# Performance work log

Measured on AMD Instinct MI355X. Metric: run time of the kernel, lower is better.

## Reference

```python
import jax, jax.numpy as jnp
import numpy as np

N_NODES = 16384
DIM = 1024
NUM_HEADS = 16
HEAD_DIM = 64
CURV = -1.0  # hyperbolic stereographic (Poincare ball) curvature, shared by all heads
EPS = 1e-15
PROJ_EPS = 4e-3  # geoopt float32 projection eps


def _clamp_abs(x, eps):
    # geoopt.utils.clamp_abs: sign-preserving clamp of |x| (sign(0) -> +1)
    s = jnp.sign(jnp.sign(x) + 0.5)
    return s * jnp.maximum(jnp.abs(x), eps)


def _artan_k(x, k):  # k < 0: artanh(sqrt(-k) x)/sqrt(-k)
    sk = jnp.sqrt(jnp.maximum(jnp.abs(k), EPS))
    return jnp.arctanh(jnp.clip(sk * x, -1.0 + 1e-7, 1.0 - 1e-7)) / sk


def _tan_k(x, k):  # k < 0: tanh(sqrt(-k) x)/sqrt(-k)
    sk = jnp.sqrt(jnp.maximum(jnp.abs(k), EPS))
    return jnp.tanh(sk * x) / sk


def _norm(x):
    return jnp.maximum(jnp.linalg.norm(x, axis=-1, keepdims=True), EPS)


def _project(x, k):
    maxnorm = (1.0 - PROJ_EPS) / jnp.sqrt(jnp.maximum(jnp.abs(k), EPS))
    n = _norm(x)
    return jnp.where(n > maxnorm, x / n * maxnorm, x)


def _mobius_scalar_mul(r, x, k):
    xn = _norm(x)
    return _tan_k(r * _artan_k(xn, k), k) * x / xn


def _mobius_matvec(W, x, k):
    xn = _norm(x)
    mx = x @ W
    mxn = _norm(mx)
    res = _tan_k(mxn / xn * _artan_k(xn, k), k) * mx / mxn
    zero = jnp.all(mx == 0, axis=-1, keepdims=True)
    return jnp.where(zero, jnp.zeros((), x.dtype), res)


def _logmap0(y, k):
    yn = _norm(y)
    return _artan_k(yn, k) * y / yn


def _expmap0(u, k):
    un = _norm(u)
    return _project(_tan_k(un, k) * u / un, k)


def _kappa_relu(x, k):
    # manifold.apply(relu): relu in tangent space at origin
    return _expmap0(jax.nn.relu(_logmap0(x, k)), k)


def _geo_lin_attn(Q, K, V, mask, k):
    # Q,K,V: (H,N,hd); mask: (N,); k: (H,1,1)
    denom_pt = jnp.maximum(1.0 + k * jnp.sum(V * V, -1, keepdims=True), EPS)  # (H,N,1)
    v1 = jax.nn.elu(Q / denom_pt) + 1.0          # parallel_transport0back(V, Q) -> elu+1
    gamma = 2.0 / denom_pt                        # lambda_x(V)
    denominator = _clamp_abs(gamma - 1.0, 1e-10)
    m = mask[None, :, None]
    x = gamma / denominator * V * m
    v2 = denominator * (jax.nn.elu(K / denom_pt) + 1.0) * m
    v2_sum = jnp.sum(v2, axis=-2)                 # (H,hd)
    D = jnp.einsum('hnd,hd->hn', v1, v2_sum)
    D_inv = 1.0 / jnp.where(D == 0, 1e-5, D)
    context = jnp.einsum('hnd,hne->hde', v2, x)   # (H,hd,hd)
    out = jnp.einsum('hde,hnd,hn->hne', context, v1, D_inv)
    out = _project(out, k)
    out = _mobius_scalar_mul(0.5, out, k)
    return _project(out, k)


def setup_inputs():
    key = jax.random.key(0)
    ks = jax.random.split(key, 6)
    kc = jnp.float32(CURV)
    X = _project(0.02 * jax.random.normal(ks[0], (N_NODES, DIM), jnp.float32), kc)
    mask = jnp.ones((N_NODES,), jnp.float32)
    hdim = NUM_HEADS * HEAD_DIM
    Wq = 0.02 * jax.random.normal(ks[1], (DIM, hdim), jnp.float32)
    bq = jnp.zeros((hdim,), jnp.float32)
    Wk = 0.02 * jax.random.normal(ks[2], (DIM, hdim), jnp.float32)
    bk = jnp.zeros((hdim,), jnp.float32)
    Wv = 0.01 * jax.random.normal(ks[3], (DIM, hdim), jnp.float32)
    Wff = 0.01 * jax.random.normal(ks[4], (hdim, DIM), jnp.float32)
    return {"X": X, "mask": mask, "Wq": Wq, "bq": bq, "Wk": Wk, "bk": bk, "Wv": Wv, "Wff": Wff}


def reference(X, mask, Wq, bq, Wk, bk, Wv, Wff):
    kc = jnp.float32(CURV)
    k_head = jnp.full((NUM_HEADS, 1, 1), CURV, X.dtype)

    def split(t):  # (N, H*hd) -> (H, N, hd)
        return t.reshape(N_NODES, NUM_HEADS, HEAD_DIM).transpose(1, 0, 2)

    Q = split(X @ Wq + bq)
    K = split(X @ Wk + bk)
    V = split(_kappa_relu(_mobius_matvec(Wv, X, kc), kc))  # KappaGCN with A_hat=None
    attn = _geo_lin_attn(Q, K, V, mask, k_head)            # (H,N,hd)
    comb = attn.transpose(1, 0, 2).reshape(N_NODES, NUM_HEADS * HEAD_DIM)
    return _kappa_relu(_mobius_matvec(Wff, comb, kc), kc)
```

## Files before the change

### kernel.cpp

```cpp
#include <hip/hip_runtime.h>
#include <hip/hip_bf16.h>
#include <math.h>

#define N_NODES 16384
#define DIMV 1024
#define NHEADS 16
#define HEADD 64

typedef __attribute__((ext_vector_type(8))) short short8;
typedef __attribute__((ext_vector_type(4))) float f32x4;
typedef unsigned short ushort_t;

#define GLD16(gptr, lptr)                                                                 \
  __builtin_amdgcn_global_load_lds((const __attribute__((address_space(1))) void*)(gptr), \
                                   (__attribute__((address_space(3))) void*)(lptr), 16, 0, 0)


__device__ __forceinline__ float waveReduceSum(float v) {
#pragma unroll
  for (int m = 32; m; m >>= 1) v += __shfl_xor(v, m);
  return v;
}

__device__ __forceinline__ float blockReduceSum(float v, float* red) {
  float w = waveReduceSum(v);
  __syncthreads();
  if ((threadIdx.x & 63) == 0) red[threadIdx.x >> 6] = w;
  __syncthreads();
  return red[0] + red[1] + red[2] + red[3];
}

__device__ __forceinline__ float elup1_fast(float z) {
  return z > 0.0f ? z + 1.0f : __expf(z);
}

__device__ __forceinline__ float clampabs(float x, float eps) {
  float s = (x >= 0.0f) ? 1.0f : -1.0f;
  return s * fmaxf(fabsf(x), eps);
}

__device__ __forceinline__ ushort_t f2b(float x) {
  unsigned u = __float_as_uint(x);
  unsigned r = (u + 0x7FFFu + ((u >> 16) & 1u)) >> 16;
  return (ushort_t)r;
}
__device__ __forceinline__ float b2f(ushort_t h) {
  return __uint_as_float(((unsigned)h) << 16);
}

__global__ __launch_bounds__(256) void cvt_norm_kernel(const float* __restrict__ src,
                                                       ushort_t* __restrict__ dst,
                                                       float* __restrict__ rowsq) {
  __shared__ float red[4];
  const int row = blockIdx.x;
  const int t = threadIdx.x;
  float4 x4 = ((const float4*)(src + (size_t)row * DIMV))[t];
  ushort_t h[4] = {f2b(x4.x), f2b(x4.y), f2b(x4.z), f2b(x4.w)};
  ((uint2*)(dst + (size_t)row * DIMV))[t] = *(uint2*)h;
  float s = x4.x * x4.x + x4.y * x4.y + x4.z * x4.z + x4.w * x4.w;
  s = blockReduceSum(s, red);
  if (t == 0) rowsq[row] = s;
}

__global__ __launch_bounds__(256) void transW_kernel(const float* __restrict__ src,
                                                     ushort_t* __restrict__ hi) {
  __shared__ float tile[32][33];
  const int bx = blockIdx.x * 32, by = blockIdx.y * 32;
  const int tx = threadIdx.x & 31, ty = threadIdx.x >> 5;
#pragma unroll
  for (int i = 0; i < 32; i += 8) tile[ty + i][tx] = src[(size_t)(by + ty + i) * DIMV + bx + tx];
  __syncthreads();
#pragma unroll
  for (int i = 0; i < 32; i += 8)
    hi[(size_t)(bx + ty + i) * DIMV + by + tx] = f2b(tile[tx][ty + i]);
}

__global__ __launch_bounds__(256) void transW3_kernel(const float* __restrict__ s0,
                                                      const float* __restrict__ s1,
                                                      const float* __restrict__ s2,
                                                      ushort_t* __restrict__ d0,
                                                      ushort_t* __restrict__ d1,
                                                      ushort_t* __restrict__ d2) {
  __shared__ float tile[32][33];
  const float* src = (blockIdx.z == 0) ? s0 : (blockIdx.z == 1) ? s1 : s2;
  ushort_t* dst = (blockIdx.z == 0) ? d0 : (blockIdx.z == 1) ? d1 : d2;
  const int bx = blockIdx.x * 32, by = blockIdx.y * 32;
  const int tx = threadIdx.x & 31, ty = threadIdx.x >> 5;
#pragma unroll
  for (int i = 0; i < 32; i += 8) tile[ty + i][tx] = src[(size_t)(by + ty + i) * DIMV + bx + tx];
  __syncthreads();
#pragma unroll
  for (int i = 0; i < 32; i += 8)
    dst[(size_t)(bx + ty + i) * DIMV + by + tx] = f2b(tile[tx][ty + i]);
}


template <int EPI, int NB>
__global__ __launch_bounds__(512, 2) void gemm_bf(const ushort_t* __restrict__ A,
                                                  const ushort_t* __restrict__ Bt,
                                                  const float* __restrict__ biasQ,
                                                  const float* __restrict__ biasK,
                                                  const float* __restrict__ denom,
                                                  const float* __restrict__ mask,
                                                  float* __restrict__ v2sum,
                                                  float* __restrict__ mxhsq,
                                                  float* __restrict__ reluhsq,
                                                  ushort_t* __restrict__ Cq,
                                                  ushort_t* __restrict__ Ck) {
  __shared__ ushort_t As[2][256 * 64];
  __shared__ ushort_t Bs[2][256 * 64];
  const int bid = blockIdx.x;
  const int nwg = NB * 64;
  const int swz = (bid & 7) * (nwg / 8) + (bid >> 3);
  const int bm = (swz / NB) * 256;
  const int bn = (swz % NB) * 256;
  const int t = threadIdx.x;
  const int w = t >> 6, lane = t & 63, l15 = lane & 15;
  const int wr = (w >> 2) * 128;
  const int wcn = (w & 3) * 64;
  const int g4 = lane >> 4;
  const int e7 = l15 & 7;
  const int uo0 = (g4 ^ e7) * 8;
  const int uo1 = ((4 + g4) ^ e7) * 8;

  const int rowin = lane >> 3;
  const int ksh = ((lane & 7) ^ ((lane >> 3) & 7)) * 8;
  const ushort_t *gA[4], *gB[4];
  int lofs[4];
#pragma unroll
  for (int c = 0; c < 4; ++c) {
    const int ch = w + 8 * c;
    lofs[c] = ch * 512;
    gA[c] = A + (size_t)(bm + ch * 8 + rowin) * DIMV + ksh;
    gB[c] = Bt + (size_t)(bn + ch * 8 + rowin) * DIMV + ksh;
  }

#define STAGE_G(buf, k0)                              \
  do {                                                \
    _Pragma("unroll") for (int c = 0; c < 4; ++c) {   \
      GLD16(gA[c] + (k0), &As[buf][lofs[c]]);         \
      GLD16(gB[c] + (k0), &Bs[buf][lofs[c]]);         \
    }                                                 \
  } while (0)

  f32x4 acc[8][4];
#pragma unroll
  for (int i = 0; i < 8; ++i)
#pragma unroll
    for (int j = 0; j < 4; ++j) acc[i][j] = (f32x4){0.f, 0.f, 0.f, 0.f};

  STAGE_G(0, 0);
  __syncthreads();
  int cur = 0;
  for (int k0 = 0; k0 < DIMV; k0 += 64) {
    if (k0 + 64 < DIMV) STAGE_G(cur ^ 1, k0 + 64);
#pragma unroll
    for (int ks = 0; ks < 2; ++ks) {
      const int uo = ks ? uo1 : uo0;
      short8 bf[4];
#pragma unroll
      for (int j = 0; j < 4; ++j)
        bf[j] = *(const short8*)&Bs[cur][(wcn + j * 16 + l15) * 64 + uo];
#pragma unroll
      for (int i = 0; i < 8; ++i) {
        short8 af = *(const short8*)&As[cur][(wr + i * 16 + l15) * 64 + uo];
#pragma unroll
        for (int j = 0; j < 4; ++j)
          acc[i][j] = __builtin_amdgcn_mfma_f32_16x16x32_bf16(af, bf[j], acc[i][j], 0, 0, 0);
      }
    }
    __syncthreads();
    cur ^= 1;
  }
#undef STAGE_G

  const int rbase = (lane >> 4) * 4;
  if (EPI == 0) {
#pragma unroll
    for (int j = 0; j < 4; ++j) {
      const int col = bn + wcn + j * 16 + l15;
#pragma unroll
      for (int i = 0; i < 8; ++i)
#pragma unroll
        for (int r = 0; r < 4; ++r)
          Cq[(size_t)(bm + wr + i * 16 + rbase + r) * DIMV + col] = f2b(acc[i][j][r]);
    }
  } else if (EPI == 4) {
    const int h = ((bn + wcn) >> 6) & (NHEADS - 1);
#pragma unroll
    for (int i = 0; i < 8; ++i) {
#pragma unroll
      for (int r = 0; r < 4; ++r) {
        const int row = bm + wr + i * 16 + rbase + r;
        float smx = 0.f, srel = 0.f;
#pragma unroll
        for (int j = 0; j < 4; ++j) {
          float val = acc[i][j][r];
          Cq[(size_t)row * DIMV + bn + wcn + j * 16 + l15] = f2b(val);
          smx = fmaf(val, val, smx);
          float rv = fmaxf(val, 0.f);
          srel = fmaf(rv, rv, srel);
        }
        smx += __shfl_xor(smx, 1); smx += __shfl_xor(smx, 2);
        smx += __shfl_xor(smx, 4); smx += __shfl_xor(smx, 8);
        srel += __shfl_xor(srel, 1); srel += __shfl_xor(srel, 2);
        srel += __shfl_xor(srel, 4); srel += __shfl_xor(srel, 8);
        if (l15 == 0) {
          mxhsq[(size_t)h * N_NODES + row] = smx;
          reluhsq[(size_t)h * N_NODES + row] = srel;
        }
      }
    }
  } else {
    const bool isK = (bn >= DIMV);
    const int h = ((bn + wcn) >> 6) & (NHEADS - 1);
    int lc[4];
    float bb[4];
#pragma unroll
    for (int j = 0; j < 4; ++j) {
      lc[j] = (bn + wcn + j * 16 + l15) & (DIMV - 1);
      bb[j] = isK ? biasK[lc[j]] : biasQ[lc[j]];
    }
    float csum[4] = {0.f, 0.f, 0.f, 0.f};
#pragma unroll
    for (int i = 0; i < 8; ++i) {
#pragma unroll
      for (int r = 0; r < 4; ++r) {
        const int row = bm + wr + i * 16 + rbase + r;
        const float invdp = 1.0f / denom[(size_t)h * N_NODES + row];
        float den = 0.f, mk = 0.f;
        if (isK) {
          den = clampabs(2.0f * invdp - 1.0f, 1e-10f);
          mk = mask[row];
        }
#pragma unroll
        for (int j = 0; j < 4; ++j) {
          float val = elup1_fast((acc[i][j][r] + bb[j]) * invdp);
          if (isK) {
            val = den * val * mk;
            csum[j] += val;
            Ck[(size_t)row * DIMV + lc[j]] = f2b(val);
          } else {
            Cq[(size_t)row * DIMV + lc[j]] = f2b(val);
          }
        }
      }
    }
    if (isK) {
#pragma unroll
      for (int j = 0; j < 4; ++j) atomicAdd(&v2sum[lc[j]], csum[j]);
    }
  }
}

__global__ __launch_bounds__(256) void vscale_kernel(const float* __restrict__ xnormsq,
                                                     const float* __restrict__ mxhsq,
                                                     const float* __restrict__ reluhsq,
                                                     float* __restrict__ scaleV,
                                                     float* __restrict__ denom) {
  const int row = blockIdx.x * 256 + threadIdx.x;
  float sm = 0.f, sr = 0.f;
  float hs[NHEADS];
#pragma unroll
  for (int h = 0; h < NHEADS; ++h) {
    sm += mxhsq[(size_t)h * N_NODES + row];
    hs[h] = reluhsq[(size_t)h * N_NODES + row];
    sr += hs[h];
  }
  float sx = xnormsq[row];
  float xn = fmaxf(sqrtf(sx), 1e-15f);
  float mxn = fmaxf(sqrtf(sm), 1e-15f);
  float cx = fminf(xn, 1.0f - 1e-7f);
  float t1 = tanhf(mxn / xn * atanhf(cx));
  float s1 = t1 / mxn;
  float yn = fmaxf(fabsf(t1), 1e-15f);
  float a = atanhf(fminf(yn, 1.0f - 1e-7f)) / yn;
  float k1 = a * s1;
  float un = fmaxf(k1 * sqrtf(sr), 1e-15f);
  float t2 = tanhf(un);
  float s2 = t2 / un;
  if (t2 > 0.996f) s2 *= 0.996f / t2;
  float sV = s2 * k1;
  scaleV[row] = sV;
#pragma unroll
  for (int h = 0; h < NHEADS; ++h)
    denom[(size_t)h * N_NODES + row] = fmaxf(1.0f - sV * sV * hs[h], 1e-15f);
}

__global__ __launch_bounds__(256) void rowtrans_kernel(const ushort_t* __restrict__ msrc,
                                                       const float* __restrict__ rowsq,
                                                       float* __restrict__ dstv) {
  __shared__ float red[4];
  const int row = blockIdx.x;
  const int t = threadIdx.x;
  uint2 mraw = ((const uint2*)(msrc + (size_t)row * DIMV))[t];
  ushort_t* mh = (ushort_t*)&mraw;
  float4 m4 = make_float4(b2f(mh[0]), b2f(mh[1]), b2f(mh[2]), b2f(mh[3]));
  float sm = m4.x * m4.x + m4.y * m4.y + m4.z * m4.z + m4.w * m4.w;
  sm = blockReduceSum(sm, red);
  float sx = rowsq[row];

  float xn = fmaxf(sqrtf(sx), 1e-15f);
  float mxn = fmaxf(sqrtf(sm), 1e-15f);
  float cx = fminf(xn, 1.0f - 1e-7f);
  float t1 = tanhf(mxn / xn * atanhf(cx));
  float s1 = t1 / mxn;

  float yn = fmaxf(fabsf(t1), 1e-15f);
  float a = atanhf(fminf(yn, 1.0f - 1e-7f)) / yn;
  float k1 = a * s1;
  float4 u = make_float4(fmaxf(k1 * m4.x, 0.0f), fmaxf(k1 * m4.y, 0.0f),
                         fmaxf(k1 * m4.z, 0.0f), fmaxf(k1 * m4.w, 0.0f));
  float su = u.x * u.x + u.y * u.y + u.z * u.z + u.w * u.w;
  su = blockReduceSum(su, red);

  float un = fmaxf(sqrtf(su), 1e-15f);
  float t2 = tanhf(un);
  float s2 = t2 / un;
  if (t2 > 0.996f) s2 *= 0.996f / t2;
  float4 o = make_float4(s2 * u.x, s2 * u.y, s2 * u.z, s2 * u.w);
  ((float4*)(dstv + (size_t)row * DIMV))[t] = o;
}

__global__ __launch_bounds__(256) void context_kernel(const ushort_t* __restrict__ v2buf,
                                                      const ushort_t* __restrict__ mxVbuf,
                                                      const float* __restrict__ scaleV,
                                                      const float* __restrict__ denom,
                                                      const float* __restrict__ mask,
                                                      float* __restrict__ ctxT) {
  __shared__ float s2[64][65];
  __shared__ float sx[64][65];
  const int h = blockIdx.y;
  const int t = threadIdx.x;
  const int d0 = (t >> 4) * 4;
  const int e0 = (t & 15) * 4;
  float acc[4][4];
#pragma unroll
  for (int i = 0; i < 4; ++i)
#pragma unroll
    for (int j = 0; j < 4; ++j) acc[i][j] = 0.0f;

  const int rbase = blockIdx.x * 512;
  for (int c = 0; c < 8; ++c) {
#pragma unroll
    for (int i = 0; i < 4; ++i) {
      int f = i * 256 + t;
      int r = f >> 4;
      int cc = (f & 15) * 4;
      int row = rbase + c * 64 + r;
      uint2 araw = *(const uint2*)(v2buf + (size_t)row * DIMV + h * HEADD + cc);
      ushort_t* ah = (ushort_t*)&araw;
      s2[r][cc + 0] = b2f(ah[0]); s2[r][cc + 1] = b2f(ah[1]);
      s2[r][cc + 2] = b2f(ah[2]); s2[r][cc + 3] = b2f(ah[3]);
      float dp = denom[(size_t)h * N_NODES + row];
      float gamma = 2.0f / dp;
      float den = clampabs(gamma - 1.0f, 1e-10f);
      float c1 = gamma / den * mask[row] * scaleV[row];
      uint2 braw = *(const uint2*)(mxVbuf + (size_t)row * DIMV + h * HEADD + cc);
      ushort_t* bh = (ushort_t*)&braw;
      sx[r][cc + 0] = c1 * fmaxf(b2f(bh[0]), 0.f); sx[r][cc + 1] = c1 * fmaxf(b2f(bh[1]), 0.f);
      sx[r][cc + 2] = c1 * fmaxf(b2f(bh[2]), 0.f); sx[r][cc + 3] = c1 * fmaxf(b2f(bh[3]), 0.f);
    }
    __syncthreads();
    for (int r = 0; r < 64; ++r) {
      float av[4], bv[4];
#pragma unroll
      for (int i = 0; i < 4; ++i) av[i] = s2[r][d0 + i];
#pragma unroll
      for (int j = 0; j < 4; ++j) bv[j] = sx[r][e0 + j];
#pragma unroll
      for (int i = 0; i < 4; ++i)
#pragma unroll
        for (int j = 0; j < 4; ++j) acc[i][j] = fmaf(av[i], bv[j], acc[i][j]);
    }
    __syncthreads();
  }
#pragma unroll
  for (int i = 0; i < 4; ++i)
#pragma unroll
    for (int j = 0; j < 4; ++j)
      atomicAdd(&ctxT[h * 4096 + (e0 + j) * 64 + (d0 + i)], acc[i][j]);
}

__global__ __launch_bounds__(256) void out_mfma_kernel(const ushort_t* __restrict__ v1bf,
                                                       const float* __restrict__ v2sum,
                                                       const float* __restrict__ ctxT,
                                                       ushort_t* __restrict__ combHi,
                                                       float* __restrict__ combnorm) {
  __shared__ ushort_t Blds[80][88];
  const int h = blockIdx.y;
  const int bm = blockIdx.x * 256;
  const int t = threadIdx.x;
  const int w = t >> 6, lane = t & 63, l15 = lane & 15;
  const int kk = (lane >> 4) * 8;

  for (int idx = t; idx < 80 * 64; idx += 256) {
    int e = idx >> 6, d = idx & 63;
    float v = 0.0f;
    if (e < 64) v = ctxT[h * 4096 + e * 64 + d];
    else if (e == 64) v = v2sum[h * 64 + d];
    Blds[e][d] = f2b(v);
  }
  __syncthreads();

  f32x4 acc[4][5];
#pragma unroll
  for (int i = 0; i < 4; ++i)
#pragma unroll
    for (int j = 0; j < 5; ++j) acc[i][j] = (f32x4){0.f, 0.f, 0.f, 0.f};
#pragma unroll
  for (int ks = 0; ks < 2; ++ks) {
    short8 bfr[5];
#pragma unroll
    for (int j = 0; j < 5; ++j) bfr[j] = *(const short8*)&Blds[j * 16 + l15][ks * 32 + kk];
#pragma unroll
    for (int i = 0; i < 4; ++i) {
      short8 af = *(const short8*)(v1bf + (size_t)(bm + w * 64 + i * 16 + l15) * DIMV +
                                   h * HEADD + ks * 32 + kk);
#pragma unroll
      for (int j = 0; j < 5; ++j)
        acc[i][j] = __builtin_amdgcn_mfma_f32_16x16x32_bf16(af, bfr[j], acc[i][j], 0, 0, 0);
    }
  }

  const int g4 = (lane >> 4) * 4;
#pragma unroll
  for (int i = 0; i < 4; ++i) {
#pragma unroll
    for (int r = 0; r < 4; ++r) {
      const int row = bm + w * 64 + i * 16 + g4 + r;
      float D = __shfl(acc[i][4][r], lane & 48);
      float Dinv = 1.0f / (D == 0.0f ? 1e-5f : D);
      float o[4];
      float s = 0.0f;
#pragma unroll
      for (int j = 0; j < 4; ++j) {
        o[j] = acc[i][j][r] * Dinv;
        s = fmaf(o[j], o[j], s);
      }
      s += __shfl_xor(s, 1); s += __shfl_xor(s, 2);
      s += __shfl_xor(s, 4); s += __shfl_xor(s, 8);
      float n1 = fmaxf(sqrtf(s), 1e-15f);
      float sc = 1.0f;
      if (n1 > 0.996f) sc = 0.996f / n1;
      float xn = fmaxf(fminf(n1, 0.996f), 1e-15f);
      float cx = fminf(xn, 1.0f - 1e-7f);
      float t2 = cx / (1.0f + sqrtf(1.0f - cx * cx));
      sc *= t2 / xn;
      if (l15 == 0) atomicAdd(&combnorm[row], s * sc * sc);
#pragma unroll
      for (int j = 0; j < 4; ++j) {
        float ov = o[j] * sc;
        combHi[(size_t)row * DIMV + h * HEADD + j * 16 + l15] = f2b(ov);
      }
    }
  }
}


extern "C" void kernel_launch(void* const* d_in, const int* in_sizes, int n_in,
                              void* d_out, int out_size, void* d_ws, size_t ws_size,
                              hipStream_t stream) {
  const float* X = (const float*)d_in[0];
  const float* mask = (const float*)d_in[1];
  const float* Wq = (const float*)d_in[2];
  const float* bq = (const float*)d_in[3];
  const float* Wk = (const float*)d_in[4];
  const float* bk = (const float*)d_in[5];
  const float* Wv = (const float*)d_in[6];
  const float* Wff = (const float*)d_in[7];
  float* out = (float*)d_out;

  const size_t MAT = (size_t)N_NODES * DIMV;
  char* p = (char*)d_ws;
  ushort_t* v1bf = (ushort_t*)p;
  ushort_t* mxV = (ushort_t*)(p + MAT * 2);
  float* combnorm = (float*)(p + MAT * 2);
  p += MAT * 4;
  float* xnormsq = (float*)p;
  ushort_t* v2bf = (ushort_t*)p;
  ushort_t* combHi = (ushort_t*)p;
  p += MAT * 4;
  ushort_t* WffHi = (ushort_t*)p;
  p += MAT * 2;
  ushort_t* Xbf = (ushort_t*)p;
  ushort_t* outBf = Xbf;
  p += MAT * 2;
  float* denom = (float*)p;   p += (size_t)NHEADS * N_NODES * 4;
  float* v2sum = (float*)p;   p += 1024 * 4;
  float* ctxT = (float*)p;    p += (size_t)NHEADS * 4096 * 4;
  float* mxhsq = (float*)p;   p += (size_t)NHEADS * N_NODES * 4;
  float* reluhsq = (float*)p; p += (size_t)NHEADS * N_NODES * 4;
  float* scaleV = (float*)p;  p += (size_t)N_NODES * 4;
  const size_t need = (size_t)(p - (char*)d_ws);
  if (ws_size < need) return;

  ushort_t* Wt = (ushort_t*)d_out;
  ushort_t* WtK = Wt + (size_t)DIMV * DIMV;
  ushort_t* WtV = WtK + (size_t)DIMV * DIMV;

  dim3 tgrid(32, 32);

  cvt_norm_kernel<<<N_NODES, 256, 0, stream>>>(X, Xbf, xnormsq);
  transW3_kernel<<<dim3(32, 32, 3), 256, 0, stream>>>(Wq, Wk, Wv, Wt, WtK, WtV);
  gemm_bf<4, 4><<<256, 512, 0, stream>>>(Xbf, WtV, nullptr, nullptr, nullptr, nullptr,
                                         nullptr, mxhsq, reluhsq, mxV, nullptr);
  vscale_kernel<<<N_NODES / 256, 256, 0, stream>>>(xnormsq, mxhsq, reluhsq, scaleV, denom);
  hipMemsetAsync(v2sum, 0, (1024 + 4096 * NHEADS) * sizeof(float), stream);
  gemm_bf<3, 8><<<512, 512, 0, stream>>>(Xbf, Wt, bq, bk, denom, mask, v2sum, nullptr,
                                         nullptr, v1bf, v2bf);
  context_kernel<<<dim3(32, NHEADS), 256, 0, stream>>>(v2bf, mxV, scaleV, denom, mask, ctxT);
  hipMemsetAsync(combnorm, 0, N_NODES * sizeof(float), stream);
  out_mfma_kernel<<<dim3(N_NODES / 256, NHEADS), 256, 0, stream>>>(v1bf, v2sum, ctxT, combHi,
                                                                   combnorm);
  transW_kernel<<<tgrid, 256, 0, stream>>>(Wff, WffHi);
  gemm_bf<0, 4><<<256, 512, 0, stream>>>(combHi, WffHi, nullptr, nullptr, nullptr, nullptr,
                                         nullptr, nullptr, nullptr, outBf, nullptr);
  rowtrans_kernel<<<N_NODES, 256, 0, stream>>>(outBf, combnorm, out);
}
```

Baseline: 370.2 us.

## Compute context outer-product accumulation with bf16 MFMA and swizzled transposed LDS

The per-head context reduction (sum over nodes of v2^T x) moves from scalar FMA on padded fp32 LDS tiles to bf16 MFMA 16x16x32 instructions. Operands are stored transposed in LDS as bf16 with an XOR swizzle so each lane can load 8 contiguous k-elements without bank conflicts. This cuts LDS footprint and ALU work for this stage. In exchange, the scaled x operand is rounded to bf16, which lowers accumulation precision.

```diff
diff --git a/kernel.cpp b/kernel.cpp
--- a/kernel.cpp
+++ b/kernel.cpp
@@ -328,17 +328,18 @@
                                                       const float* __restrict__ denom,
                                                       const float* __restrict__ mask,
                                                       float* __restrict__ ctxT) {
-  __shared__ float s2[64][65];
-  __shared__ float sx[64][65];
+  __shared__ ushort_t s2T[64 * 64];
+  __shared__ ushort_t sxT[64 * 64];
   const int h = blockIdx.y;
   const int t = threadIdx.x;
-  const int d0 = (t >> 4) * 4;
-  const int e0 = (t & 15) * 4;
-  float acc[4][4];
-#pragma unroll
-  for (int i = 0; i < 4; ++i)
-#pragma unroll
-    for (int j = 0; j < 4; ++j) acc[i][j] = 0.0f;
+  const int w = t >> 6, lane = t & 63, l15 = lane & 15, g = lane >> 4;
+  const int e7 = l15 & 7;
+  const int uo0 = (g ^ e7) * 8;
+  const int uo1 = ((4 + g) ^ e7) * 8;
+
+  f32x4 acc[4];
+#pragma unroll
+  for (int j = 0; j < 4; ++j) acc[j] = (f32x4){0.f, 0.f, 0.f, 0.f};
 
   const int rbase = blockIdx.x * 512;
   for (int c = 0; c < 8; ++c) {
@@ -350,36 +351,39 @@
       int row = rbase + c * 64 + r;
       uint2 araw = *(const uint2*)(v2buf + (size_t)row * DIMV + h * HEADD + cc);
       ushort_t* ah = (ushort_t*)&araw;
-      s2[r][cc + 0] = b2f(ah[0]); s2[r][cc + 1] = b2f(ah[1]);
-      s2[r][cc + 2] = b2f(ah[2]); s2[r][cc + 3] = b2f(ah[3]);
       float dp = denom[(size_t)h * N_NODES + row];
       float gamma = 2.0f / dp;
       float den = clampabs(gamma - 1.0f, 1e-10f);
       float c1 = gamma / den * mask[row] * scaleV[row];
       uint2 braw = *(const uint2*)(mxVbuf + (size_t)row * DIMV + h * HEADD + cc);
       ushort_t* bh = (ushort_t*)&braw;
-      sx[r][cc + 0] = c1 * fmaxf(b2f(bh[0]), 0.f); sx[r][cc + 1] = c1 * fmaxf(b2f(bh[1]), 0.f);
-      sx[r][cc + 2] = c1 * fmaxf(b2f(bh[2]), 0.f); sx[r][cc + 3] = c1 * fmaxf(b2f(bh[3]), 0.f);
+      const int rhi = r >> 3, rlo = r & 7;
+#pragma unroll
+      for (int q = 0; q < 4; ++q) {
+        const int d = cc + q;
+        const int pos = d * 64 + ((rhi ^ (d & 7)) << 3) + rlo;
+        s2T[pos] = ah[q];
+        sxT[pos] = f2b(c1 * fmaxf(b2f(bh[q]), 0.f));
+      }
     }
     __syncthreads();
-    for (int r = 0; r < 64; ++r) {
-      float av[4], bv[4];
-#pragma unroll
-      for (int i = 0; i < 4; ++i) av[i] = s2[r][d0 + i];
-#pragma unroll
-      for (int j = 0; j < 4; ++j) bv[j] = sx[r][e0 + j];
-#pragma unroll
-      for (int i = 0; i < 4; ++i)
-#pragma unroll
-        for (int j = 0; j < 4; ++j) acc[i][j] = fmaf(av[i], bv[j], acc[i][j]);
+#pragma unroll
+    for (int ks = 0; ks < 2; ++ks) {
+      const int uo = ks ? uo1 : uo0;
+      short8 af = *(const short8*)&s2T[(w * 16 + l15) * 64 + uo];
+#pragma unroll
+      for (int j = 0; j < 4; ++j) {
+        short8 bfv = *(const short8*)&sxT[(j * 16 + l15) * 64 + uo];
+        acc[j] = __builtin_amdgcn_mfma_f32_16x16x32_bf16(af, bfv, acc[j], 0, 0, 0);
+      }
     }
     __syncthreads();
   }
 #pragma unroll
-  for (int i = 0; i < 4; ++i)
-#pragma unroll
-    for (int j = 0; j < 4; ++j)
-      atomicAdd(&ctxT[h * 4096 + (e0 + j) * 64 + (d0 + i)], acc[i][j]);
+  for (int j = 0; j < 4; ++j)
+#pragma unroll
+    for (int r = 0; r < 4; ++r)
+      atomicAdd(&ctxT[h * 4096 + (j * 16 + l15) * 64 + w * 16 + g * 4 + r], acc[j][r]);
 }
 
 __global__ __launch_bounds__(256) void out_mfma_kernel(const ushort_t* __restrict__ v1bf,
```

New measurement: 350.2 us. -5.4%, faster.
